# Performance work log

Hardware: AMD Instinct MI355X
Metric: run time of the kernel (lower is better)

The kernel has to match this reference:

```python
import jax, jax.numpy as jnp
import numpy as np

N = 524288      # total trajectory tokens
D_MODEL = 256
HIDDEN = 512
OUT_DIM = 32
N_TYPES = 4


def setup_inputs() -> dict:
    key = jax.random.key(0)
    k1, k2, k3, k4 = jax.random.split(key, 4)
    x = jax.random.normal(k1, (N, D_MODEL), dtype=jnp.float32)
    types = jax.random.randint(k2, (N,), 0, N_TYPES, dtype=jnp.int64)
    W1 = jax.random.normal(k3, (N_TYPES, D_MODEL, HIDDEN), dtype=jnp.float32) / np.sqrt(D_MODEL)
    b1 = jnp.zeros((N_TYPES, HIDDEN), dtype=jnp.float32)
    W2 = jax.random.normal(k4, (N_TYPES, HIDDEN, OUT_DIM), dtype=jnp.float32) / np.sqrt(HIDDEN)
    b2 = jnp.zeros((N_TYPES, OUT_DIM), dtype=jnp.float32)
    return {"x": x, "types": types, "W1": W1, "b1": b1, "W2": W2, "b2": b2}


def reference(x, types, W1, b1, W2, b2):
    # Type-masked gather -> per-type MLP decode -> scatter back to original order.
    # The gather/argsort-scatter of the torch code is equivalent (for equal
    # per-type output dims) to computing each type's decoder and selecting the
    # rows where types == type_id; we loop over the small fixed set of types.
    n_types = W1.shape[0]
    out = jnp.zeros((x.shape[0], W2.shape[-1]), dtype=x.dtype)
    for t in range(n_types):
        h = jax.nn.relu(x @ W1[t] + b1[t])          # [N, HIDDEN]
        y = h @ W2[t] + b2[t]                        # [N, OUT_DIM]
        out = jnp.where((types == t)[:, None], y, out)
    return out
```

## Files before the change

kernel.cpp:

```cpp
#include <hip/hip_runtime.h>
#include <hip/hip_bf16.h>
#include <hip/hip_fp16.h>

#define N_TOK 524288
#define DM 256
#define HID 512
#define OUTD 32
#define NTYPE 4
#define BM 128
#define MT 2
#define HC 32
#define NCHUNK (HID / HC)
#define CHUNK_BYTES (HC * DM * 2)
#define NBLK 512
#define GX1D (N_TOK / BM + NTYPE)

typedef _Float16 half8 __attribute__((ext_vector_type(8)));
typedef float f32x4 __attribute__((ext_vector_type(4)));


__global__ void count_kernel(const int* __restrict__ types, int* __restrict__ bc) {
    __shared__ int c[NTYPE];
    int tid = threadIdx.x;
    if (tid < NTYPE) c[tid] = 0;
    __syncthreads();
    int b = blockIdx.x;
    int lane = tid & 63;
    #pragma unroll
    for (int j = 0; j < 4; ++j) {
        int t = types[b * 1024 + j * 256 + tid];
        #pragma unroll
        for (int tt = 0; tt < NTYPE; ++tt) {
            unsigned long long mask = __ballot(t == tt);
            if (lane == 0) atomicAdd(&c[tt], __popcll(mask));
        }
    }
    __syncthreads();
    if (tid < NTYPE) bc[tid * NBLK + b] = c[tid];
}

__global__ void scan_blocks_kernel(const int* __restrict__ bc,
                                   int* __restrict__ bb,
                                   int* __restrict__ meta) {
    __shared__ int totals[NTYPE];
    __shared__ int typeoff[NTYPE];
    int wave = threadIdx.x >> 6, lane = threadIdx.x & 63;
    int excl[NBLK / 64];
    int running = 0;
    #pragma unroll
    for (int it = 0; it < NBLK / 64; ++it) {
        int v = bc[wave * NBLK + it * 64 + lane];
        int s = v;
        #pragma unroll
        for (int d = 1; d < 64; d <<= 1) {
            int u = __shfl_up(s, d);
            if (lane >= d) s += u;
        }
        excl[it] = running + s - v;
        running += __shfl(s, 63);
    }
    if (lane == 0) totals[wave] = running;
    __syncthreads();
    if (threadIdx.x == 0) {
        int off = 0, toff = 0;
        for (int tt = 0; tt < NTYPE; ++tt) {
            typeoff[tt] = off;
            meta[tt] = totals[tt];
            meta[4 + tt] = off;
            meta[8 + tt] = toff;
            off += totals[tt];
            toff += (totals[tt] + BM - 1) / BM;
        }
        meta[12] = toff;
    }
    __syncthreads();
    #pragma unroll
    for (int it = 0; it < NBLK / 64; ++it)
        bb[wave * NBLK + it * 64 + lane] = typeoff[wave] + excl[it];
}

__global__ void scatter2_kernel(const int* __restrict__ types,
                                const int* __restrict__ bb,
                                int* __restrict__ idx) {
    __shared__ int base[NTYPE];
    __shared__ int wcnt[4][NTYPE];
    int b = blockIdx.x;
    int tid = threadIdx.x, wave = tid >> 6, lane = tid & 63;
    if (tid < NTYPE) base[tid] = bb[tid * NBLK + b];
    #pragma unroll
    for (int j = 0; j < 4; ++j) {
        __syncthreads();
        int i = b * 1024 + j * 256 + tid;
        int t = types[i];
        int rank = 0;
        #pragma unroll
        for (int tt = 0; tt < NTYPE; ++tt) {
            unsigned long long mask = __ballot(t == tt);
            if (t == tt) rank = __popcll(mask & ((1ull << lane) - 1ull));
            if (lane == 0) wcnt[wave][tt] = __popcll(mask);
        }
        __syncthreads();
        int pre = 0;
        for (int w = 0; w < wave; ++w) pre += wcnt[w][t];
        idx[base[t] + pre + rank] = i;
        __syncthreads();
        if (tid < NTYPE) {
            int tot = 0;
            #pragma unroll
            for (int w = 0; w < 4; ++w) tot += wcnt[w][tid];
            base[tid] += tot;
        }
    }
}


__global__ void wprep_kernel(const float* __restrict__ W1, const float* __restrict__ W2,
                             _Float16* __restrict__ W1T, _Float16* __restrict__ W2T) {
    int i = blockIdx.x * blockDim.x + threadIdx.x;
    if (i < NTYPE * HID * DM) {
        int t = i / (HID * DM);
        int r = i - t * (HID * DM);
        int byteoff = r * 2;
        int hc = byteoff / CHUNK_BYTES;
        int rem = byteoff - hc * CHUNK_BYTES;
        int hr = rem >> 9;
        int brow = rem & 511;
        int d = (brow ^ ((hr & 7) << 4)) >> 1;
        int h = hc * HC + hr;
        W1T[i] = (_Float16)W1[(t * DM + d) * HID + h];
    }
    if (i < NTYPE * OUTD * HID) {
        int t = i / (OUTD * HID);
        int r = i - t * (OUTD * HID);
        int o = r / HID;
        int pg = r - o * HID;
        int hc = pg >> 5;
        int p = pg & 31;
        int lg = p >> 3, j = p & 7;
        int h1 = (j < 4) ? (lg * 4 + j) : (16 + lg * 4 + (j - 4));
        int h = hc * HC + h1;
        W2T[i] = (_Float16)W2[(t * HID + h) * OUTD + o];
    }
}


__launch_bounds__(256)
__global__ void fused_mlp_kernel(const float* __restrict__ x,
                                 const int* __restrict__ meta,
                                 const int* __restrict__ idx,
                                 const _Float16* __restrict__ W1T,
                                 const _Float16* __restrict__ W2T,
                                 const float* __restrict__ b1,
                                 const float* __restrict__ b2,
                                 float* __restrict__ out) {
    const int b = blockIdx.x;
    if (b >= meta[12]) return;
    const int t = (b >= meta[9]) + (b >= meta[10]) + (b >= meta[11]);
    const int cnt = meta[t];
    const int row_base = (b - meta[8 + t]) * BM;
    const int* idx_t = idx + meta[4 + t];

    __shared__ __align__(16) char W1sB[2][CHUNK_BYTES];
    __shared__ __align__(16) float b1s[HID];

    const int tid = threadIdx.x;
    const int wave = tid >> 6;
    const int lane = tid & 63;
    const int l15 = lane & 15;
    const int lg = lane >> 4;

    {
        float2 bv = *(const float2*)(b1 + t * HID + tid * 2);
        b1s[tid * 2] = bv.x;
        b1s[tid * 2 + 1] = bv.y;
    }

    half8 afrag[MT][8];
    #pragma unroll
    for (int mt = 0; mt < MT; ++mt) {
        int rl = wave * (MT * 16) + mt * 16 + l15;
        int rglob = idx_t[min(row_base + rl, cnt - 1)];
        const float* xr = x + (size_t)rglob * DM;
        #pragma unroll
        for (int kk = 0; kk < 8; ++kk) {
            int k0 = kk * 32 + lg * 8;
            f32x4 v0 = __builtin_nontemporal_load((const f32x4*)(xr + k0));
            f32x4 v1 = __builtin_nontemporal_load((const f32x4*)(xr + k0 + 4));
            half8 h;
            h[0] = (_Float16)v0[0]; h[1] = (_Float16)v0[1];
            h[2] = (_Float16)v0[2]; h[3] = (_Float16)v0[3];
            h[4] = (_Float16)v1[0]; h[5] = (_Float16)v1[1];
            h[6] = (_Float16)v1[2]; h[7] = (_Float16)v1[3];
            afrag[mt][kk] = h;
        }
    }

    const f32x4 fzero = {0.f, 0.f, 0.f, 0.f};
    f32x4 acc2[MT][2];
    #pragma unroll
    for (int mt = 0; mt < MT; ++mt)
        #pragma unroll
        for (int nt = 0; nt < 2; ++nt)
            acc2[mt][nt] = fzero;

    const char* w1base = (const char*)(W1T + (size_t)t * HID * DM);
    const _Float16* w2t_t = W2T + (size_t)t * OUTD * HID;

    #pragma unroll
    for (int it = 0; it < 4; ++it) {
        __builtin_amdgcn_global_load_lds(
            (const __attribute__((address_space(1))) void*)(w1base + it * 4096 + tid * 16),
            (__attribute__((address_space(3))) void*)(&W1sB[0][it * 4096 + tid * 16]),
            16, 0, 0);
    }
    half8 w2A[2], w2B[2];
    #pragma unroll
    for (int nt = 0; nt < 2; ++nt)
        w2A[nt] = *(const half8*)(w2t_t + (nt * 16 + l15) * HID + lg * 8);
    __syncthreads();

#define CHUNK_BODY(HCI, W2USE, W2FILL)                                          \
    {                                                                           \
        const int hc = (HCI);                                                   \
        const char* cur = W1sB[hc & 1];                                         \
        if (hc + 1 < NCHUNK) {                                                  \
            const char* src = w1base + (size_t)(hc + 1) * CHUNK_BYTES;          \
            char* dst = W1sB[(hc + 1) & 1];                                     \
            _Pragma("unroll")                                                   \
            for (int it = 0; it < 4; ++it) {                                    \
                __builtin_amdgcn_global_load_lds(                               \
                    (const __attribute__((address_space(1))) void*)(src + it * 4096 + tid * 16), \
                    (__attribute__((address_space(3))) void*)(dst + it * 4096 + tid * 16),       \
                    16, 0, 0);                                                  \
            }                                                                   \
        }                                                                       \
        {                 \
            int hn = (hc + 1) & 15;                                             \
            _Pragma("unroll")                                                   \
            for (int nt = 0; nt < 2; ++nt)                                      \
                W2FILL[nt] = *(const half8*)(w2t_t + (nt * 16 + l15) * HID + hn * HC + lg * 8); \
        }                                                                       \
        f32x4 acc1[MT][2];    \
        _Pragma("unroll")                                                       \
        for (int mt = 0; mt < MT; ++mt)                                         \
            _Pragma("unroll")                                                   \
            for (int nt = 0; nt < 2; ++nt)                                      \
                acc1[mt][nt] = fzero;                                           \
        _Pragma("unroll")                                                       \
        for (int kk = 0; kk < 8; ++kk) {                                        \
            half8 bfr[2];                                                       \
            _Pragma("unroll")                                                   \
            for (int nt = 0; nt < 2; ++nt) {                                    \
                int hr = nt * 16 + l15;                                         \
                bfr[nt] = *(const half8*)(cur + hr * 512 +                      \
                            ((kk * 64 + lg * 16) ^ ((hr & 7) << 4)));           \
            }                                                                   \
            _Pragma("unroll")                                                   \
            for (int mt = 0; mt < MT; ++mt)                                     \
                _Pragma("unroll")                                               \
                for (int nt = 0; nt < 2; ++nt)                                  \
                    acc1[mt][nt] = __builtin_amdgcn_mfma_f32_16x16x32_f16(      \
                        bfr[nt], afrag[mt][kk], acc1[mt][nt], 0, 0, 0);         \
        }                                                                       \
              \
        {                                                                       \
            f32x4 bv0 = *(const f32x4*)(b1s + hc * HC + lg * 4);                \
            f32x4 bv1 = *(const f32x4*)(b1s + hc * HC + 16 + lg * 4);           \
            _Pragma("unroll")                                                   \
            for (int mt = 0; mt < MT; ++mt) {                                   \
                half8 hfrag;                                                    \
                _Pragma("unroll")                                               \
                for (int j = 0; j < 4; ++j) {                                   \
                    hfrag[j]     = (_Float16)fmaxf(acc1[mt][0][j] + bv0[j], 0.f);\
                    hfrag[4 + j] = (_Float16)fmaxf(acc1[mt][1][j] + bv1[j], 0.f);\
                }                                                               \
                _Pragma("unroll")                                               \
                for (int nt = 0; nt < 2; ++nt)                                  \
                    acc2[mt][nt] = __builtin_amdgcn_mfma_f32_16x16x32_f16(      \
                        W2USE[nt], hfrag, acc2[mt][nt], 0, 0, 0);               \
            }                                                                   \
        }                                                                       \
        __syncthreads();   \
    }

    #pragma unroll
    for (int h2 = 0; h2 < NCHUNK; h2 += 2) {
        CHUNK_BODY(h2, w2A, w2B);
        CHUNK_BODY(h2 + 1, w2B, w2A);
    }
#undef CHUNK_BODY

    const int m = min(BM, cnt - row_base);
    f32x4 b2v[2];
    #pragma unroll
    for (int nt = 0; nt < 2; ++nt)
        b2v[nt] = *(const f32x4*)(b2 + t * OUTD + nt * 16 + lg * 4);
    #pragma unroll
    for (int mt = 0; mt < MT; ++mt) {
        int rloc = wave * (MT * 16) + mt * 16 + l15;
        if (rloc < m) {
            int gr = idx_t[row_base + rloc];
            #pragma unroll
            for (int nt = 0; nt < 2; ++nt) {
                f32x4 v = acc2[mt][nt] + b2v[nt];
                __builtin_nontemporal_store(v, (f32x4*)(out + (size_t)gr * OUTD + nt * 16 + lg * 4));
            }
        }
    }
}


extern "C" void kernel_launch(void* const* d_in, const int* in_sizes, int n_in,
                              void* d_out, int out_size, void* d_ws, size_t ws_size,
                              hipStream_t stream) {
    const float* x   = (const float*)d_in[0];
    const int* types = (const int*)d_in[1];
    const float* W1  = (const float*)d_in[2];
    const float* b1  = (const float*)d_in[3];
    const float* W2  = (const float*)d_in[4];
    const float* b2  = (const float*)d_in[5];
    float* out = (float*)d_out;

    char* ws = (char*)d_ws;
    int* meta = (int*)ws;
    int* idx = (int*)(ws + 64);
    _Float16* W1T = (_Float16*)(ws + 64 + 4 * (size_t)N_TOK);
    _Float16* W2T = W1T + (size_t)NTYPE * HID * DM;
    int* bc = (int*)W1T;
    int* bb = bc + NTYPE * NBLK;

    count_kernel<<<NBLK, 256, 0, stream>>>(types, bc);
    scan_blocks_kernel<<<1, 256, 0, stream>>>(bc, bb, meta);
    scatter2_kernel<<<NBLK, 256, 0, stream>>>(types, bb, idx);
    wprep_kernel<<<(NTYPE * HID * DM) / 256, 256, 0, stream>>>(W1, W2, W1T, W2T);

    fused_mlp_kernel<<<GX1D, 256, 0, stream>>>(x, meta, idx, W1T, W2T, b1, b2, out);
}
```

Baseline: 254.1 us.

## Stage gathered x rows through LDS with async global_load_lds double buffering

Replaces the per-lane strided gather of x rows, in which each lane loaded fragments straight from global memory, with whole-row async global_load_lds copies into a per-wave LDS scratch (reusing the W1 buffer). Row indices are preloaded into registers, and groups of 4 rows are double-buffered with manual vmcnt waits. Lanes then read rotated offsets from LDS to build the fp16 A fragments. The aim is fully coalesced, deeper-in-flight loads for the gather phase, at the cost of extra LDS traffic, 32 index registers and a block-wide sync before W1 streaming starts.

After: 233.4 us. -8.2%, faster.

```diff
diff --git a/kernel.cpp b/kernel.cpp
--- a/kernel.cpp
+++ b/kernel.cpp
@@ -17,6 +17,9 @@
 
 typedef _Float16 half8 __attribute__((ext_vector_type(8)));
 typedef float f32x4 __attribute__((ext_vector_type(4)));
+
+#define AS1 __attribute__((address_space(1)))
+#define AS3 __attribute__((address_space(3)))
 
 
 __global__ void count_kernel(const int* __restrict__ types, int* __restrict__ bc) {
@@ -174,26 +177,60 @@
         b1s[tid * 2] = bv.x;
         b1s[tid * 2 + 1] = bv.y;
     }
+    __builtin_amdgcn_sched_barrier(0);
+
+    int rg[32];
+    #pragma unroll
+    for (int r = 0; r < 32; ++r)
+        rg[r] = idx_t[min(row_base + wave * 32 + r, cnt - 1)];
+    __builtin_amdgcn_sched_barrier(0);
 
     half8 afrag[MT][8];
-    #pragma unroll
-    for (int mt = 0; mt < MT; ++mt) {
-        int rl = wave * (MT * 16) + mt * 16 + l15;
-        int rglob = idx_t[min(row_base + rl, cnt - 1)];
-        const float* xr = x + (size_t)rglob * DM;
-        #pragma unroll
-        for (int kk = 0; kk < 8; ++kk) {
-            int k0 = kk * 32 + lg * 8;
-            f32x4 v0 = __builtin_nontemporal_load((const f32x4*)(xr + k0));
-            f32x4 v1 = __builtin_nontemporal_load((const f32x4*)(xr + k0 + 4));
-            half8 h;
-            h[0] = (_Float16)v0[0]; h[1] = (_Float16)v0[1];
-            h[2] = (_Float16)v0[2]; h[3] = (_Float16)v0[3];
-            h[4] = (_Float16)v1[0]; h[5] = (_Float16)v1[1];
-            h[6] = (_Float16)v1[2]; h[7] = (_Float16)v1[3];
-            afrag[mt][kk] = h;
-        }
-    }
+    char* scratch = &W1sB[0][0] + wave * 8192;
+
+#define ISSUE_GROUP(G)                                                          \
+    {                                                                           \
+        _Pragma("unroll")                                                       \
+        for (int i = 0; i < 4; ++i) {                                           \
+            const char* src = (const char*)(x + (size_t)rg[(G) * 4 + i] * DM)   \
+                              + ((lane - i) & 63) * 16;                         \
+            __builtin_amdgcn_global_load_lds(                                   \
+                (const AS1 void*)src,                                           \
+                (AS3 void*)(scratch + ((G) & 1) * 4096 + i * 1024), 16, 0, 0);  \
+        }                                                                       \
+    }
+
+    ISSUE_GROUP(0)
+#define GATHER_GROUP(G)                                                         \
+    {                                                                           \
+        if ((G) < 7) { __builtin_amdgcn_sched_barrier(0); ISSUE_GROUP((G) + 1) }\
+        if ((G) < 7) asm volatile("s_waitcnt vmcnt(4)");                        \
+        else         asm volatile("s_waitcnt vmcnt(0)");                        \
+        __builtin_amdgcn_sched_barrier(0);                                      \
+        if ((l15 >> 2) == ((G) & 3)) {                                          \
+            const int r3 = l15 & 3;                                             \
+            const char* gb = scratch + ((G) & 1) * 4096 + r3 * 1024;            \
+            _Pragma("unroll")                                                   \
+            for (int kk = 0; kk < 8; ++kk) {                                    \
+                int B0 = kk * 128 + lg * 32;                                    \
+                f32x4 v0 = *(const f32x4*)(gb + ((B0 + r3 * 16) & 1023));       \
+                f32x4 v1 = *(const f32x4*)(gb + ((B0 + 16 + r3 * 16) & 1023));  \
+                half8 h;                                                        \
+                h[0] = (_Float16)v0[0]; h[1] = (_Float16)v0[1];                 \
+                h[2] = (_Float16)v0[2]; h[3] = (_Float16)v0[3];                 \
+                h[4] = (_Float16)v1[0]; h[5] = (_Float16)v1[1];                 \
+                h[6] = (_Float16)v1[2]; h[7] = (_Float16)v1[3];                 \
+                afrag[(G) >> 2][kk] = h;                                        \
+            }                                                                   \
+        }                                                                       \
+    }
+
+    GATHER_GROUP(0) GATHER_GROUP(1) GATHER_GROUP(2) GATHER_GROUP(3)
+    GATHER_GROUP(4) GATHER_GROUP(5) GATHER_GROUP(6) GATHER_GROUP(7)
+#undef GATHER_GROUP
+#undef ISSUE_GROUP
+
+    __syncthreads();
 
     const f32x4 fzero = {0.f, 0.f, 0.f, 0.f};
     f32x4 acc2[MT][2];
@@ -209,8 +246,8 @@
     #pragma unroll
     for (int it = 0; it < 4; ++it) {
         __builtin_amdgcn_global_load_lds(
-            (const __attribute__((address_space(1))) void*)(w1base + it * 4096 + tid * 16),
-            (__attribute__((address_space(3))) void*)(&W1sB[0][it * 4096 + tid * 16]),
+            (const AS1 void*)(w1base + it * 4096 + tid * 16),
+            (AS3 void*)(&W1sB[0][it * 4096 + tid * 16]),
             16, 0, 0);
     }
     half8 w2A[2], w2B[2];
@@ -229,8 +266,8 @@
             _Pragma("unroll")                                                   \
             for (int it = 0; it < 4; ++it) {                                    \
                 __builtin_amdgcn_global_load_lds(                               \
-                    (const __attribute__((address_space(1))) void*)(src + it * 4096 + tid * 16), \
-                    (__attribute__((address_space(3))) void*)(dst + it * 4096 + tid * 16),       \
+                    (const AS1 void*)(src + it * 4096 + tid * 16),              \
+                    (AS3 void*)(dst + it * 4096 + tid * 16),                    \
                     16, 0, 0);                                                  \
             }                                                                   \
         }                                                                       \
```

## Make fused MLP persistent and prefetch next tile's x rows during compute

Applied to the files above, without the earlier changes.

The fused MLP kernel becomes persistent: 512 blocks loop over tiles with a stride of the grid size instead of launching one block per tile. While the current tile's hidden chunks are computed, the gathered x rows for the next tile are streamed into per-wave LDS scratch with global_load_lds and converted to fp16 fragments, along with that tile's first W1 chunk, W2 fragments and b1. This is meant to hide the gather latency of x and the per-block startup cost behind MFMA work. In exchange it raises register pressure, since two sets of A fragments are held at once, and uses more LDS, which may lower occupancy.

New measurement: 373.4 us (median of 2 runs). +46.9%, slower.

```diff
diff --git a/kernel.cpp b/kernel.cpp
--- a/kernel.cpp
+++ b/kernel.cpp
@@ -13,10 +13,13 @@
 #define NCHUNK (HID / HC)
 #define CHUNK_BYTES (HC * DM * 2)
 #define NBLK 512
-#define GX1D (N_TOK / BM + NTYPE)
+#define GRID_X 512
 
 typedef _Float16 half8 __attribute__((ext_vector_type(8)));
 typedef float f32x4 __attribute__((ext_vector_type(4)));
+
+#define AS1 __attribute__((address_space(1)))
+#define AS3 __attribute__((address_space(3)))
 
 
 __global__ void count_kernel(const int* __restrict__ types, int* __restrict__ bc) {
@@ -153,47 +156,111 @@
                                  const float* __restrict__ b1,
                                  const float* __restrict__ b2,
                                  float* __restrict__ out) {
-    const int b = blockIdx.x;
-    if (b >= meta[12]) return;
-    const int t = (b >= meta[9]) + (b >= meta[10]) + (b >= meta[11]);
-    const int cnt = meta[t];
-    const int row_base = (b - meta[8 + t]) * BM;
-    const int* idx_t = idx + meta[4 + t];
-
     __shared__ __align__(16) char W1sB[2][CHUNK_BYTES];
-    __shared__ __align__(16) float b1s[HID];
+    __shared__ __align__(16) char scr[4][2][2048];
+    __shared__ __align__(16) float b1s[2][HID];
+    __shared__ int idsL[4][32];
+
+    const int ntiles = meta[12];
+    int tile = blockIdx.x;
+    if (tile >= ntiles) return;
 
     const int tid = threadIdx.x;
     const int wave = tid >> 6;
     const int lane = tid & 63;
     const int l15 = lane & 15;
     const int lg = lane >> 4;
-
-    {
-        float2 bv = *(const float2*)(b1 + t * HID + tid * 2);
-        b1s[tid * 2] = bv.x;
-        b1s[tid * 2 + 1] = bv.y;
-    }
-
-    half8 afrag[MT][8];
-    #pragma unroll
-    for (int mt = 0; mt < MT; ++mt) {
-        int rl = wave * (MT * 16) + mt * 16 + l15;
-        int rglob = idx_t[min(row_base + rl, cnt - 1)];
-        const float* xr = x + (size_t)rglob * DM;
-        #pragma unroll
-        for (int kk = 0; kk < 8; ++kk) {
-            int k0 = kk * 32 + lg * 8;
-            f32x4 v0 = __builtin_nontemporal_load((const f32x4*)(xr + k0));
-            f32x4 v1 = __builtin_nontemporal_load((const f32x4*)(xr + k0 + 4));
-            half8 h;
-            h[0] = (_Float16)v0[0]; h[1] = (_Float16)v0[1];
-            h[2] = (_Float16)v0[2]; h[3] = (_Float16)v0[3];
-            h[4] = (_Float16)v1[0]; h[5] = (_Float16)v1[1];
-            h[6] = (_Float16)v1[2]; h[7] = (_Float16)v1[3];
-            afrag[mt][kk] = h;
-        }
-    }
+    char* myScr = &scr[wave][0][0];
+
+    int tC = (tile >= meta[9]) + (tile >= meta[10]) + (tile >= meta[11]);
+    int cntC = meta[tC];
+    int rbaseC = (tile - meta[8 + tC]) * BM;
+    const int* idxC = idx + meta[4 + tC];
+    const char* w1C = (const char*)(W1T + (size_t)tC * HID * DM);
+    const _Float16* w2C = W2T + (size_t)tC * OUTD * HID;
+
+    int tileN = tile + GRID_X;
+    bool hasNext = tileN < ntiles;
+    int tN = 0, cntN = 1, rbaseN = 0;
+    const int* idxN = idx;
+    const char* w1N = w1C;
+    const _Float16* w2N = w2C;
+    const float* b1N = b1;
+    if (hasNext) {
+        tN = (tileN >= meta[9]) + (tileN >= meta[10]) + (tileN >= meta[11]);
+        cntN = meta[tN];
+        rbaseN = (tileN - meta[8 + tN]) * BM;
+        idxN = idx + meta[4 + tN];
+        w1N = (const char*)(W1T + (size_t)tN * HID * DM);
+        w2N = W2T + (size_t)tN * OUTD * HID;
+        b1N = b1 + tN * HID;
+    }
+
+    half8 afragC[MT][8], afragN[MT][8];
+
+#define GISSUE(P)                                                               \
+    {                                                                           \
+        int2 rid = *(const int2*)&idsL[wave][2 * (P)];                          \
+        const char* s0 = (const char*)(x + (size_t)rid.x * DM) + lane * 16;     \
+        const char* s1 = (const char*)(x + (size_t)rid.y * DM)                  \
+                         + ((lane - 1) & 63) * 16;                              \
+        __builtin_amdgcn_global_load_lds((const AS1 void*)s0,                   \
+            (AS3 void*)(myScr + ((P) & 1) * 2048 + lane * 16), 16, 0, 0);       \
+        __builtin_amdgcn_global_load_lds((const AS1 void*)s1,                   \
+            (AS3 void*)(myScr + ((P) & 1) * 2048 + 1024 + lane * 16), 16, 0, 0);\
+    }
+
+#define REDIST(P, DEST)                                                         \
+    {                                                                           \
+        if ((l15 & 14) == ((2 * (P)) & 15)) {                                   \
+            const int rsel = l15 & 1;                                           \
+            const char* gb = myScr + ((P) & 1) * 2048 + rsel * 1024;            \
+            _Pragma("unroll")                                                   \
+            for (int kk = 0; kk < 8; ++kk) {                                    \
+                int B0 = kk * 128 + lg * 32 + rsel * 16;                        \
+                f32x4 v0 = *(const f32x4*)(gb + (B0 & 1023));                   \
+                f32x4 v1 = *(const f32x4*)(gb + ((B0 + 16) & 1023));            \
+                half8 h;                                                        \
+                h[0] = (_Float16)v0[0]; h[1] = (_Float16)v0[1];                 \
+                h[2] = (_Float16)v0[2]; h[3] = (_Float16)v0[3];                 \
+                h[4] = (_Float16)v1[0]; h[5] = (_Float16)v1[1];                 \
+                h[6] = (_Float16)v1[2]; h[7] = (_Float16)v1[3];                 \
+                DEST[(P) >> 3][kk] = h;                                         \
+            }                                                                   \
+        }                                                                       \
+    }
+
+    if (lane < 32)
+        idsL[wave][lane] = idxC[min(rbaseC + wave * 32 + lane, cntC - 1)];
+    GISSUE(0)
+#define PSTEP(P)                                                                \
+    __builtin_amdgcn_sched_barrier(0);                                          \
+    GISSUE(P)                                                                   \
+    __builtin_amdgcn_sched_barrier(0);                                          \
+    asm volatile("s_waitcnt vmcnt(2)");                                         \
+    __builtin_amdgcn_sched_barrier(0);                                          \
+    REDIST((P) - 1, afragC)
+    PSTEP(1) PSTEP(2) PSTEP(3) PSTEP(4) PSTEP(5) PSTEP(6) PSTEP(7)
+    PSTEP(8) PSTEP(9) PSTEP(10) PSTEP(11) PSTEP(12) PSTEP(13) PSTEP(14) PSTEP(15)
+#undef PSTEP
+
+    if (hasNext && lane < 32)
+        idsL[wave][lane] = idxN[min(rbaseN + wave * 32 + lane, cntN - 1)];
+
+    #pragma unroll
+    for (int it = 0; it < 4; ++it)
+        __builtin_amdgcn_global_load_lds(
+            (const AS1 void*)(w1C + it * 4096 + tid * 16),
+            (AS3 void*)(&W1sB[0][it * 4096 + tid * 16]), 16, 0, 0);
+    if (wave < 2)
+        __builtin_amdgcn_global_load_lds(
+            (const AS1 void*)((const char*)(b1 + tC * HID) + tid * 16),
+            (AS3 void*)((char*)&b1s[0][0] + tid * 16), 16, 0, 0);
+    half8 w2A[2], w2B[2];
+    #pragma unroll
+    for (int nt = 0; nt < 2; ++nt)
+        w2A[nt] = *(const half8*)(w2C + (nt * 16 + l15) * HID + lg * 8);
+    __syncthreads();
 
     const f32x4 fzero = {0.f, 0.f, 0.f, 0.f};
     f32x4 acc2[MT][2];
@@ -203,49 +270,50 @@
         for (int nt = 0; nt < 2; ++nt)
             acc2[mt][nt] = fzero;
 
-    const char* w1base = (const char*)(W1T + (size_t)t * HID * DM);
-    const _Float16* w2t_t = W2T + (size_t)t * OUTD * HID;
-
-    #pragma unroll
-    for (int it = 0; it < 4; ++it) {
-        __builtin_amdgcn_global_load_lds(
-            (const __attribute__((address_space(1))) void*)(w1base + it * 4096 + tid * 16),
-            (__attribute__((address_space(3))) void*)(&W1sB[0][it * 4096 + tid * 16]),
-            16, 0, 0);
-    }
-    half8 w2A[2], w2B[2];
-    #pragma unroll
-    for (int nt = 0; nt < 2; ++nt)
-        w2A[nt] = *(const half8*)(w2t_t + (nt * 16 + l15) * HID + lg * 8);
-    __syncthreads();
-
-#define CHUNK_BODY(HCI, W2USE, W2FILL)                                          \
+    int par = 0;
+
+#define CHUNK_BODY(I, W2USE, W2FILL)                                            \
     {                                                                           \
-        const int hc = (HCI);                                                   \
-        const char* cur = W1sB[hc & 1];                                         \
-        if (hc + 1 < NCHUNK) {                                                  \
-            const char* src = w1base + (size_t)(hc + 1) * CHUNK_BYTES;          \
-            char* dst = W1sB[(hc + 1) & 1];                                     \
-            _Pragma("unroll")                                                   \
-            for (int it = 0; it < 4; ++it) {                                    \
+        if ((I) == 0 && hasNext && wave < 2)                                    \
+            __builtin_amdgcn_global_load_lds(                                   \
+                (const AS1 void*)((const char*)b1N + tid * 16),                 \
+                (AS3 void*)((char*)&b1s[par ^ 1][0] + tid * 16), 16, 0, 0);     \
+        if ((I) == 0) { REDIST(15, afragC) }                                    \
+        else if (hasNext) { REDIST((I) - 1, afragN) }                           \
+        if ((I) < 15) {                                                         \
+            const char* srcw = w1C + (size_t)((I) + 1) * CHUNK_BYTES;           \
+            char* dstw = W1sB[((I) + 1) & 1];                                   \
+            _Pragma("unroll")                                                   \
+            for (int it = 0; it < 4; ++it)                                      \
                 __builtin_amdgcn_global_load_lds(                               \
-                    (const __attribute__((address_space(1))) void*)(src + it * 4096 + tid * 16), \
-                    (__attribute__((address_space(3))) void*)(dst + it * 4096 + tid * 16),       \
-                    16, 0, 0);                                                  \
-            }                                                                   \
+                    (const AS1 void*)(srcw + it * 4096 + tid * 16),             \
+                    (AS3 void*)(dstw + it * 4096 + tid * 16), 16, 0, 0);        \
+        } else if (hasNext) {                                                   \
+            char* dstw = W1sB[0];                                               \
+            _Pragma("unroll")                                                   \
+            for (int it = 0; it < 4; ++it)                                      \
+                __builtin_amdgcn_global_load_lds(                               \
+                    (const AS1 void*)(w1N + it * 4096 + tid * 16),              \
+                    (AS3 void*)(dstw + it * 4096 + tid * 16), 16, 0, 0);        \
         }                                                                       \
-        {                 \
-            int hn = (hc + 1) & 15;                                             \
+        if (hasNext) { GISSUE(I) }                                              \
+        if ((I) < 15) {                                                         \
             _Pragma("unroll")                                                   \
             for (int nt = 0; nt < 2; ++nt)                                      \
-                W2FILL[nt] = *(const half8*)(w2t_t + (nt * 16 + l15) * HID + hn * HC + lg * 8); \
+                W2FILL[nt] = *(const half8*)(w2C + (nt * 16 + l15) * HID        \
+                                             + ((I) + 1) * HC + lg * 8);        \
+        } else if (hasNext) {                                                   \
+            _Pragma("unroll")                                                   \
+            for (int nt = 0; nt < 2; ++nt)                                      \
+                W2FILL[nt] = *(const half8*)(w2N + (nt * 16 + l15) * HID + lg * 8); \
         }                                                                       \
-        f32x4 acc1[MT][2];    \
+        f32x4 acc1[MT][2];                                                      \
         _Pragma("unroll")                                                       \
         for (int mt = 0; mt < MT; ++mt)                                         \
             _Pragma("unroll")                                                   \
             for (int nt = 0; nt < 2; ++nt)                                      \
                 acc1[mt][nt] = fzero;                                           \
+        const char* cur = W1sB[(I) & 1];                                        \
         _Pragma("unroll")                                                       \
         for (int kk = 0; kk < 8; ++kk) {                                        \
             half8 bfr[2];                                                       \
@@ -260,12 +328,11 @@
                 _Pragma("unroll")                                               \
                 for (int nt = 0; nt < 2; ++nt)                                  \
                     acc1[mt][nt] = __builtin_amdgcn_mfma_f32_16x16x32_f16(      \
-                        bfr[nt], afrag[mt][kk], acc1[mt][nt], 0, 0, 0);         \
+                        bfr[nt], afragC[mt][kk], acc1[mt][nt], 0, 0, 0);        \
         }                                                                       \
-              \
         {                                                                       \
-            f32x4 bv0 = *(const f32x4*)(b1s + hc * HC + lg * 4);                \
-            f32x4 bv1 = *(const f32x4*)(b1s + hc * HC + 16 + lg * 4);           \
+            f32x4 bv0 = *(const f32x4*)(&b1s[par][(I) * HC + lg * 4]);          \
+            f32x4 bv1 = *(const f32x4*)(&b1s[par][(I) * HC + 16 + lg * 4]);     \
             _Pragma("unroll")                                                   \
             for (int mt = 0; mt < MT; ++mt) {                                   \
                 half8 hfrag;                                                    \
@@ -280,33 +347,73 @@
                         W2USE[nt], hfrag, acc2[mt][nt], 0, 0, 0);               \
             }                                                                   \
         }                                                                       \
-        __syncthreads();   \
-    }
-
-    #pragma unroll
-    for (int h2 = 0; h2 < NCHUNK; h2 += 2) {
-        CHUNK_BODY(h2, w2A, w2B);
-        CHUNK_BODY(h2 + 1, w2B, w2A);
+        __syncthreads();                                                        \
+    }
+
+    for (;;) {
+        CHUNK_BODY(0,  w2A, w2B)  CHUNK_BODY(1,  w2B, w2A)
+        CHUNK_BODY(2,  w2A, w2B)  CHUNK_BODY(3,  w2B, w2A)
+        CHUNK_BODY(4,  w2A, w2B)  CHUNK_BODY(5,  w2B, w2A)
+        CHUNK_BODY(6,  w2A, w2B)  CHUNK_BODY(7,  w2B, w2A)
+        CHUNK_BODY(8,  w2A, w2B)  CHUNK_BODY(9,  w2B, w2A)
+        CHUNK_BODY(10, w2A, w2B)  CHUNK_BODY(11, w2B, w2A)
+        CHUNK_BODY(12, w2A, w2B)  CHUNK_BODY(13, w2B, w2A)
+        CHUNK_BODY(14, w2A, w2B)  CHUNK_BODY(15, w2B, w2A)
+
+        {
+            const int m = min(BM, cntC - rbaseC);
+            f32x4 b2v[2];
+            #pragma unroll
+            for (int nt = 0; nt < 2; ++nt)
+                b2v[nt] = *(const f32x4*)(b2 + tC * OUTD + nt * 16 + lg * 4);
+            #pragma unroll
+            for (int mt = 0; mt < MT; ++mt) {
+                int rloc = wave * 32 + mt * 16 + l15;
+                int gr = idxC[min(rbaseC + rloc, cntC - 1)];
+                if (rloc < m) {
+                    #pragma unroll
+                    for (int nt = 0; nt < 2; ++nt) {
+                        f32x4 v = acc2[mt][nt] + b2v[nt];
+                        __builtin_nontemporal_store(
+                            v, (f32x4*)(out + (size_t)gr * OUTD + nt * 16 + lg * 4));
+                    }
+                }
+            }
+            #pragma unroll
+            for (int mt = 0; mt < MT; ++mt)
+                #pragma unroll
+                for (int nt = 0; nt < 2; ++nt)
+                    acc2[mt][nt] = fzero;
+        }
+
+        if (!hasNext) break;
+
+        tC = tN; cntC = cntN; rbaseC = rbaseN;
+        idxC = idxN; w1C = w1N; w2C = w2N;
+        par ^= 1;
+        tileN += GRID_X;
+        hasNext = tileN < ntiles;
+        if (hasNext) {
+            tN = (tileN >= meta[9]) + (tileN >= meta[10]) + (tileN >= meta[11]);
+            cntN = meta[tN];
+            rbaseN = (tileN - meta[8 + tN]) * BM;
+            idxN = idx + meta[4 + tN];
+            w1N = (const char*)(W1T + (size_t)tN * HID * DM);
+            w2N = W2T + (size_t)tN * OUTD * HID;
+            b1N = b1 + tN * HID;
+            if (lane < 32)
+                idsL[wave][lane] = idxN[min(rbaseN + wave * 32 + lane, cntN - 1)];
+        }
+
+        #pragma unroll
+        for (int mt = 0; mt < MT; ++mt)
+            #pragma unroll
+            for (int kk = 0; kk < 8; ++kk)
+                afragC[mt][kk] = afragN[mt][kk];
     }
 #undef CHUNK_BODY
-
-    const int m = min(BM, cnt - row_base);
-    f32x4 b2v[2];
-    #pragma unroll
-    for (int nt = 0; nt < 2; ++nt)
-        b2v[nt] = *(const f32x4*)(b2 + t * OUTD + nt * 16 + lg * 4);
-    #pragma unroll
-    for (int mt = 0; mt < MT; ++mt) {
-        int rloc = wave * (MT * 16) + mt * 16 + l15;
-        if (rloc < m) {
-            int gr = idx_t[row_base + rloc];
-            #pragma unroll
-            for (int nt = 0; nt < 2; ++nt) {
-                f32x4 v = acc2[mt][nt] + b2v[nt];
-                __builtin_nontemporal_store(v, (f32x4*)(out + (size_t)gr * OUTD + nt * 16 + lg * 4));
-            }
-        }
-    }
+#undef GISSUE
+#undef REDIST
 }
 
 
@@ -334,5 +441,5 @@
     scatter2_kernel<<<NBLK, 256, 0, stream>>>(types, bb, idx);
     wprep_kernel<<<(NTYPE * HID * DM) / 256, 256, 0, stream>>>(W1, W2, W1T, W2T);
 
-    fused_mlp_kernel<<<GX1D, 256, 0, stream>>>(x, meta, idx, W1T, W2T, b1, b2, out);
-}
+    fused_mlp_kernel<<<GRID_X, 256, 0, stream>>>(x, meta, idx, W1T, W2T, b1, b2, out);
+}
```

## Stage gathered x rows through LDS with pipelined global_load_lds before fragment build

Applied to the files above, without the earlier changes.

Replaces the per-lane direct global loads of gathered x rows with whole-row global_load_lds transfers into a per-wave LDS scratch (reusing the W1 buffer), pipelined three groups deep with explicit vmcnt waits. Lanes then redistribute the rows from LDS into fp16 A fragments, using a lane-rotated layout to avoid bank conflicts. The aim is fully coalesced 1KB row reads in place of scattered 32-byte per-lane accesses for the gather. In exchange it adds LDS traffic, divergent redistribution branches and an extra block barrier before the W1 prefetch.

New measurement: 240.1 us. 1.06x faster.

```diff
diff --git a/kernel.cpp b/kernel.cpp
--- a/kernel.cpp
+++ b/kernel.cpp
@@ -17,6 +17,9 @@
 
 typedef _Float16 half8 __attribute__((ext_vector_type(8)));
 typedef float f32x4 __attribute__((ext_vector_type(4)));
+
+#define AS1 __attribute__((address_space(1)))
+#define AS3 __attribute__((address_space(3)))
 
 
 __global__ void count_kernel(const int* __restrict__ types, int* __restrict__ bc) {
@@ -174,26 +177,68 @@
         b1s[tid * 2] = bv.x;
         b1s[tid * 2 + 1] = bv.y;
     }
+    __builtin_amdgcn_sched_barrier(0);
+
+    int rg[32];
+    #pragma unroll
+    for (int r = 0; r < 32; ++r)
+        rg[r] = idx_t[min(row_base + wave * 32 + r, cnt - 1)];
+    __builtin_amdgcn_sched_barrier(0);
 
     half8 afrag[MT][8];
-    #pragma unroll
-    for (int mt = 0; mt < MT; ++mt) {
-        int rl = wave * (MT * 16) + mt * 16 + l15;
-        int rglob = idx_t[min(row_base + rl, cnt - 1)];
-        const float* xr = x + (size_t)rglob * DM;
-        #pragma unroll
-        for (int kk = 0; kk < 8; ++kk) {
-            int k0 = kk * 32 + lg * 8;
-            f32x4 v0 = __builtin_nontemporal_load((const f32x4*)(xr + k0));
-            f32x4 v1 = __builtin_nontemporal_load((const f32x4*)(xr + k0 + 4));
-            half8 h;
-            h[0] = (_Float16)v0[0]; h[1] = (_Float16)v0[1];
-            h[2] = (_Float16)v0[2]; h[3] = (_Float16)v0[3];
-            h[4] = (_Float16)v1[0]; h[5] = (_Float16)v1[1];
-            h[6] = (_Float16)v1[2]; h[7] = (_Float16)v1[3];
-            afrag[mt][kk] = h;
-        }
-    }
+    char* scratch = &W1sB[0][0] + wave * 8192;
+
+#define G2_ISSUE(G)                                                            \
+    {                                                                          \
+        _Pragma("unroll")                                                      \
+        for (int i = 0; i < 2; ++i) {                                          \
+            int r = 2 * (G) + i;                                               \
+            const char* src = (const char*)(x + (size_t)rg[r] * DM)            \
+                              + ((lane - r) & 63) * 16;                        \
+            __builtin_amdgcn_global_load_lds(                                  \
+                (const AS1 void*)src,                                          \
+                (AS3 void*)(scratch + ((G) & 3) * 2048 + i * 1024 + lane * 16),\
+                16, 0, 0);                                                     \
+        }                                                                      \
+    }
+
+#define G2_REDIST(G)                                                           \
+    if ((l15 >> 1) == ((G) & 7)) {                                             \
+        const int p = l15 & 1;                                                 \
+        const int r = 2 * (G) + p;                                             \
+        const char* gb = scratch + ((G) & 3) * 2048 + p * 1024;                \
+        _Pragma("unroll")                                                      \
+        for (int kk = 0; kk < 8; ++kk) {                                       \
+            int B0 = kk * 128 + lg * 32 + r * 16;                              \
+            f32x4 v0 = *(const f32x4*)(gb + (B0 & 1023));                      \
+            f32x4 v1 = *(const f32x4*)(gb + ((B0 + 16) & 1023));               \
+            half8 h;                                                           \
+            h[0] = (_Float16)v0[0]; h[1] = (_Float16)v0[1];                    \
+            h[2] = (_Float16)v0[2]; h[3] = (_Float16)v0[3];                    \
+            h[4] = (_Float16)v1[0]; h[5] = (_Float16)v1[1];                    \
+            h[6] = (_Float16)v1[2]; h[7] = (_Float16)v1[3];                    \
+            afrag[(G) >> 3][kk] = h;                                           \
+        }                                                                      \
+    }
+
+#define G2_STEP(G, VN)                                                         \
+    __builtin_amdgcn_sched_barrier(0);                                         \
+    if ((G) + 3 < 16) { G2_ISSUE((G) + 3) }                                    \
+    __builtin_amdgcn_sched_barrier(0);                                         \
+    asm volatile("s_waitcnt vmcnt(" #VN ")");                                  \
+    __builtin_amdgcn_sched_barrier(0);                                         \
+    G2_REDIST(G)
+
+    G2_ISSUE(0) G2_ISSUE(1) G2_ISSUE(2)
+    G2_STEP(0, 6)  G2_STEP(1, 6)  G2_STEP(2, 6)  G2_STEP(3, 6)
+    G2_STEP(4, 6)  G2_STEP(5, 6)  G2_STEP(6, 6)  G2_STEP(7, 6)
+    G2_STEP(8, 6)  G2_STEP(9, 6)  G2_STEP(10, 6) G2_STEP(11, 6)
+    G2_STEP(12, 6) G2_STEP(13, 4) G2_STEP(14, 2) G2_STEP(15, 0)
+#undef G2_STEP
+#undef G2_REDIST
+#undef G2_ISSUE
+
+    __syncthreads();
 
     const f32x4 fzero = {0.f, 0.f, 0.f, 0.f};
     f32x4 acc2[MT][2];
@@ -209,8 +254,8 @@
     #pragma unroll
     for (int it = 0; it < 4; ++it) {
         __builtin_amdgcn_global_load_lds(
-            (const __attribute__((address_space(1))) void*)(w1base + it * 4096 + tid * 16),
-            (__attribute__((address_space(3))) void*)(&W1sB[0][it * 4096 + tid * 16]),
+            (const AS1 void*)(w1base + it * 4096 + tid * 16),
+            (AS3 void*)(&W1sB[0][it * 4096 + tid * 16]),
             16, 0, 0);
     }
     half8 w2A[2], w2B[2];
@@ -229,8 +274,8 @@
             _Pragma("unroll")                                                   \
             for (int it = 0; it < 4; ++it) {                                    \
                 __builtin_amdgcn_global_load_lds(                               \
-                    (const __attribute__((address_space(1))) void*)(src + it * 4096 + tid * 16), \
-                    (__attribute__((address_space(3))) void*)(dst + it * 4096 + tid * 16),       \
+                    (const AS1 void*)(src + it * 4096 + tid * 16),              \
+                    (AS3 void*)(dst + it * 4096 + tid * 16),                    \
                     16, 0, 0);                                                  \
             }                                                                   \
         }                                                                       \
```
